# Optimization experiments

Measured on AMD Instinct MI355X. Metric: run time of the kernel, lower is better.

## Reference

```python
import jax, jax.numpy as jnp
import numpy as np

B, T, Q, H = 128, 50, 1024, 256
MAX_STEP = 50
TEMP = 0.5
SUP_W, DIST_W, EMBED_W, LOSS_WEIGHT = 1.0, 0.01, 1.0, 1.0
BLUR, DIAMETER, REACH, SCALING, P = 0.005, 1.0, 500.0, 0.5, 2
NEG = -1e9


def _softmin(eps, C, h):
    # h: log-weights + potential/eps over the second axis of C
    return -eps * jax.nn.logsumexp(h[None, :] - C / eps, axis=1)


def _sqcost(u, v):
    sq = jnp.sum(u * u, -1)[:, None] + jnp.sum(v * v, -1)[None, :] - 2.0 * (u @ v.T)
    return 0.5 * jnp.maximum(sq, 0.0)  # geomloss p=2 cost: |x-y|^2 / 2


def sinkhorn_divergence(x, y):
    # geomloss SamplesLoss('sinkhorn', p=2, blur=0.005, diameter=1, reach=500),
    # tensorized, debiased, unbalanced, eps-scaling schedule.
    N, M = x.shape[0], y.shape[0]
    a_log = jnp.full((N,), -np.log(float(N)), dtype=x.dtype)
    b_log = jnp.full((M,), -np.log(float(M)), dtype=x.dtype)
    Cxy, Cyx = _sqcost(x, y), _sqcost(y, x)
    Cxx, Cyy = _sqcost(x, x), _sqcost(y, y)
    rho = REACH ** P
    eps_final = BLUR ** P
    eps_list = []
    e = DIAMETER ** P
    while e > eps_final:
        eps_list.append(e)
        e = e * (SCALING ** P)
    eps_list.append(eps_final)
    f_ab = jnp.zeros((N,), x.dtype)
    g_ab = jnp.zeros((M,), x.dtype)
    f_aa = jnp.zeros((N,), x.dtype)
    g_bb = jnp.zeros((M,), x.dtype)
    for eps in eps_list:  # static schedule (~9 steps)
        damp = 1.0 / (1.0 + eps / rho)
        ft = damp * _softmin(eps, Cxy, b_log + g_ab / eps)
        gt = damp * _softmin(eps, Cyx, a_log + f_ab / eps)
        faa = 0.5 * (f_aa + damp * _softmin(eps, Cxx, a_log + f_aa / eps))
        gbb = 0.5 * (g_bb + damp * _softmin(eps, Cyy, b_log + g_bb / eps))
        f_ab, g_ab, f_aa, g_bb = ft, gt, faa, gbb
    w = rho + eps_final / 2.0  # UnbalancedWeight
    a_w, b_w = jnp.exp(a_log), jnp.exp(b_log)
    return (jnp.sum(a_w * w * (jnp.exp(-f_aa / rho) - jnp.exp(-f_ab / rho)))
            + jnp.sum(b_w * w * (jnp.exp(-g_bb / rho) - jnp.exp(-g_ab / rho))))


def _forward(lc, lt, le, ltc, ltt, lte, ohs, oht, ods, odt, batch):
    p_c, p_t, p_e = lc / TEMP, lt / TEMP, le / TEMP
    q_c, q_t, q_e = ltc / TEMP, ltt / TEMP, lte / TEMP
    flat = lambda z: z.reshape(z.shape[0], -1)
    loss_kd = (sinkhorn_divergence(flat(p_c), flat(q_c))
               + sinkhorn_divergence(flat(p_t), flat(q_t))
               + sinkhorn_divergence(flat(p_e), flat(q_e)))
    S = MAX_STEP - 1
    delta = batch[:, :, :Q] + batch[:, :, Q:]  # [B,T,Q] question one-hots
    a = jnp.floor(((batch[:, :, :Q] - batch[:, :, Q:]).sum(-1) + 1.0) / 2.0)[:, 1:1 + S]  # [B,S] correctness
    dsh = delta[:, 1:1 + S]  # [B,S,Q]
    # diagonal of p[:S] @ delta[1:].T == per-step gather of next question's logit
    pc = jnp.einsum('bsq,bsq->bs', p_c[:, :S], dsh)
    pt = jnp.einsum('bsq,bsq->bs', p_t[:, :S], dsh)
    pe = jnp.einsum('bsq,bsq->bs', p_e[:, :S], dsh)
    idx = jnp.arange(S)
    last = jnp.max(jnp.where(pc > 0, idx[None, :], -1), axis=1)  # last i with pc[i] > 0
    L = jnp.where(last >= 0, last + 1, S)  # no break => keep full length
    mask = idx[None, :] < L[:, None]
    def ce(logits):
        m = jnp.where(mask, logits, NEG)
        lsm = m - jax.nn.logsumexp(m, axis=1, keepdims=True)
        return -jnp.sum(jnp.where(mask, a * lsm, 0.0))  # soft-target CE, summed over students
    loss_sup = ce(pt) + ce(pc) + ce(pe)
    embed = 0.5 * (jnp.sum((ohs - oht) ** 2) + jnp.sum((ods - odt) ** 2))
    total = LOSS_WEIGHT * (SUP_W * loss_sup + DIST_W * loss_kd + EMBED_W * embed)
    return total.reshape(1)


def setup_inputs():
    key = jax.random.key(0)
    ks = jax.random.split(key, 12)
    rn = lambda k, s: jax.random.normal(k, s, dtype=jnp.float32)
    qid = jax.random.randint(ks[10], (B, T), 0, Q)
    correct = jax.random.randint(ks[11], (B, T), 0, 2).astype(jnp.float32)
    oh = jax.nn.one_hot(qid, Q, dtype=jnp.float32)
    batch = jnp.concatenate([oh * correct[..., None], oh * (1.0 - correct)[..., None]], axis=-1)
    return {
        'logit_c': rn(ks[0], (B, T, Q)),
        'logit_t': rn(ks[1], (B, T, Q)),
        'logit_ensemble': rn(ks[2], (B, T, Q)),
        'logit_teacher_c': rn(ks[3], (B, T, Q)),
        'logit_teacher_t': rn(ks[4], (B, T, Q)),
        'logit_teacher_ensemble': rn(ks[5], (B, T, Q)),
        'out_h_student': rn(ks[6], (B, T, H)),
        'out_h_teacher': rn(ks[7], (B, T, H)),
        'out_d_student': rn(ks[8], (B, T, H)),
        'out_d_teacher': rn(ks[9], (B, T, H)),
        'batch': batch,
    }


def reference(logit_c, logit_t, logit_ensemble, logit_teacher_c, logit_teacher_t, logit_teacher_ensemble, out_h_student, out_h_teacher, out_d_student, out_d_teacher, batch):
    return _forward(logit_c, logit_t, logit_ensemble, logit_teacher_c, logit_teacher_t, logit_teacher_ensemble, out_h_student, out_h_teacher, out_d_student, out_d_teacher, batch)
```

## Files before the change

kernel.cpp:

```cpp
#include <hip/hip_runtime.h>

#define NB 128
#define T_DIM 50
#define Q_DIM 1024
#define H_DIM 256
#define S_DIM 49
#define K_DIM 51200
#define KCHUNKS 80
#define KC 640
#define BK 64
#define NSTAGE 10
#define GRAM_N (NB * NB)
#define LROWU 36
#define CPAD 132

typedef __attribute__((ext_vector_type(4))) float f32x4;
typedef __attribute__((ext_vector_type(8))) _Float16 half8v;
typedef __attribute__((ext_vector_type(4))) unsigned int uint4v;
typedef __attribute__((ext_vector_type(2))) unsigned int uint2v;
using pk2_t = decltype(__builtin_amdgcn_cvt_pkrtz(0.0f, 0.0f));

union PKU { pk2_t p; unsigned int u; };
union U4H8 { uint4v u; half8v h; };

__device__ inline unsigned short f2bf_rn(float x) {
  union { float f; unsigned int u; } v; v.f = x;
  unsigned int r = v.u + 0x7FFFu + ((v.u >> 16) & 1u);
  return (unsigned short)(r >> 16);
}
__device__ inline float bf2f(unsigned short b) {
  union { float f; unsigned int u; } v; v.u = ((unsigned int)b) << 16;
  return v.f;
}

__global__ __launch_bounds__(1024) void gram_fused_kernel(
    const float* __restrict__ s0, const float* __restrict__ s1, const float* __restrict__ s2,
    const float* __restrict__ t0, const float* __restrict__ t1, const float* __restrict__ t2,
    unsigned short* __restrict__ part) {
  __shared__ unsigned int pan[2][2][NB * LROWU];

  const int chunk = blockIdx.x;
  const int pair = blockIdx.y;
  const float* S  = (pair == 0) ? s0 : ((pair == 1) ? s1 : s2);
  const float* Tm = (pair == 0) ? t0 : ((pair == 1) ? t1 : t2);

  const int tid = threadIdx.x;
  const int wave = tid >> 6, lane = tid & 63;
  const int wrow = wave >> 2, wcol = wave & 3;
  const int l15 = lane & 15, quad = lane >> 4;

  f32x4 aXY[2][2], aXX[2][2], aYY[2][2];
#pragma unroll
  for (int i = 0; i < 2; i++)
#pragma unroll
    for (int j = 0; j < 2; j++) {
      aXY[i][j] = (f32x4){0.f, 0.f, 0.f, 0.f};
      aXX[i][j] = (f32x4){0.f, 0.f, 0.f, 0.f};
      aYY[i][j] = (f32x4){0.f, 0.f, 0.f, 0.f};
    }

  const int r0 = tid >> 4;
  const int kq = tid & 15;
  const size_t ro0 = (size_t)r0 * K_DIM;
  const size_t ro1 = (size_t)(r0 + 64) * K_DIM;

  const int kbase = chunk * KC;
  f32x4 pre0, pre1, pre2, pre3;

#define ISSUE_LOADS(KPOS)                                    \
  {                                                          \
    const float* pS = S + (KPOS) + kq * 4;                   \
    const float* pT = Tm + (KPOS) + kq * 4;                  \
    pre0 = *(const f32x4*)(pS + ro0);                        \
    pre1 = *(const f32x4*)(pS + ro1);                        \
    pre2 = *(const f32x4*)(pT + ro0);                        \
    pre3 = *(const f32x4*)(pT + ro1);                        \
  }

#define CVT_WRITE(BUF)                                       \
  {                                                          \
    unsigned int* panA = &pan[BUF][0][0];                    \
    unsigned int* panB = &pan[BUF][1][0];                    \
    PKU a, b; uint2v w;                                      \
    a.p = __builtin_amdgcn_cvt_pkrtz(pre0[0], pre0[1]);      \
    b.p = __builtin_amdgcn_cvt_pkrtz(pre0[2], pre0[3]);      \
    w.x = a.u; w.y = b.u;                                    \
    *(uint2v*)&panA[r0 * LROWU + kq * 2] = w;                \
    a.p = __builtin_amdgcn_cvt_pkrtz(pre1[0], pre1[1]);      \
    b.p = __builtin_amdgcn_cvt_pkrtz(pre1[2], pre1[3]);      \
    w.x = a.u; w.y = b.u;                                    \
    *(uint2v*)&panA[(r0 + 64) * LROWU + kq * 2] = w;         \
    a.p = __builtin_amdgcn_cvt_pkrtz(pre2[0], pre2[1]);      \
    b.p = __builtin_amdgcn_cvt_pkrtz(pre2[2], pre2[3]);      \
    w.x = a.u; w.y = b.u;                                    \
    *(uint2v*)&panB[r0 * LROWU + kq * 2] = w;                \
    a.p = __builtin_amdgcn_cvt_pkrtz(pre3[0], pre3[1]);      \
    b.p = __builtin_amdgcn_cvt_pkrtz(pre3[2], pre3[3]);      \
    w.x = a.u; w.y = b.u;                                    \
    *(uint2v*)&panB[(r0 + 64) * LROWU + kq * 2] = w;         \
  }

  ISSUE_LOADS(kbase)
  CVT_WRITE(0)
  __syncthreads();

  for (int st = 0; st < NSTAGE; st++) {
    const int buf = st & 1;
    if (st + 1 < NSTAGE) ISSUE_LOADS(kbase + (st + 1) * BK)

    {
      const unsigned int* panA = &pan[buf][0][0];
      const unsigned int* panB = &pan[buf][1][0];
#pragma unroll
      for (int ks = 0; ks < 2; ks++) {
        const int kc = ks * 16 + quad * 4;
        half8v as_[2], bs_[2], at_[2], bt_[2];
#pragma unroll
        for (int t = 0; t < 2; t++) {
          U4H8 u;
          u.u = *(const uint4v*)&panA[(wrow * 32 + t * 16 + l15) * LROWU + kc]; as_[t] = u.h;
          u.u = *(const uint4v*)&panA[(wcol * 32 + t * 16 + l15) * LROWU + kc]; bs_[t] = u.h;
          u.u = *(const uint4v*)&panB[(wrow * 32 + t * 16 + l15) * LROWU + kc]; at_[t] = u.h;
          u.u = *(const uint4v*)&panB[(wcol * 32 + t * 16 + l15) * LROWU + kc]; bt_[t] = u.h;
        }
#pragma unroll
        for (int ti = 0; ti < 2; ti++)
#pragma unroll
          for (int tj = 0; tj < 2; tj++) {
            aXY[ti][tj] = __builtin_amdgcn_mfma_f32_16x16x32_f16(as_[ti], bt_[tj], aXY[ti][tj], 0, 0, 0);
            aXX[ti][tj] = __builtin_amdgcn_mfma_f32_16x16x32_f16(as_[ti], bs_[tj], aXX[ti][tj], 0, 0, 0);
            aYY[ti][tj] = __builtin_amdgcn_mfma_f32_16x16x32_f16(at_[ti], bt_[tj], aYY[ti][tj], 0, 0, 0);
          }
      }
    }

    if (st + 1 < NSTAGE) {
      CVT_WRITE((st + 1) & 1)
      __syncthreads();
    }
  }
#undef ISSUE_LOADS
#undef CVT_WRITE

#pragma unroll
  for (int kind = 0; kind < 3; kind++) {
    unsigned short* out = part + ((size_t)(pair * 3 + kind) * KCHUNKS + chunk) * GRAM_N;
#pragma unroll
    for (int ti = 0; ti < 2; ti++)
#pragma unroll
      for (int tj = 0; tj < 2; tj++) {
        const f32x4 v = (kind == 0) ? aXY[ti][tj] : ((kind == 1) ? aXX[ti][tj] : aYY[ti][tj]);
        const int col = wcol * 32 + tj * 16 + l15;
#pragma unroll
        for (int r = 0; r < 4; r++) {
          const int row = wrow * 32 + ti * 16 + quad * 4 + r;
          out[(size_t)row * NB + col] = f2bf_rn(v[r]);
        }
      }
  }
}

__global__ __launch_bounds__(256) void gram_reduce_kernel(
    const unsigned short* __restrict__ part, float* __restrict__ gram) {
  const int idx = blockIdx.x * 256 + threadIdx.x;
  const int g = idx >> 14;
  const int cell = idx & (GRAM_N - 1);
  const unsigned short* p = part + (size_t)g * KCHUNKS * GRAM_N + cell;
  float s = 0.f;
#pragma unroll
  for (int c = 0; c < KCHUNKS; c++) s += bf2f(p[(size_t)c * GRAM_N]);
  gram[idx] = s;
}

__global__ __launch_bounds__(256, 1) void sinkhorn_part_kernel(
    const float* __restrict__ gram, float* __restrict__ kdpart) {
  const int pair = blockIdx.x, kind = blockIdx.y;
  const float* Gxy = gram + (size_t)(3 * pair + 0) * GRAM_N;
  const float* Gxx = gram + (size_t)(3 * pair + 1) * GRAM_N;
  const float* Gyy = gram + (size_t)(3 * pair + 2) * GRAM_N;

  __shared__ float CL[NB * CPAD];
  __shared__ f32x4 h4a[NB / 4];
  __shared__ f32x4 h4b[NB / 4];
  __shared__ float nx[NB], ny[NB];
  __shared__ float red[256];

  const int tid = threadIdx.x;
  if (tid < NB) {
    nx[tid] = Gxx[tid * (NB + 1)];
    ny[tid] = Gyy[tid * (NB + 1)];
    ((float*)h4a)[tid] = 0.f;
    ((float*)h4b)[tid] = 0.f;
  }
  __syncthreads();

  const float* G  = (kind == 0) ? Gxy : ((kind == 1) ? Gxx : Gyy);
  const float* rn = (kind == 2) ? ny : nx;
  const float* cn = (kind == 1) ? nx : ny;
  for (int idx = tid; idx < GRAM_N; idx += 256) {
    const int i = idx >> 7, j = idx & 127;
    CL[i * CPAD + j] = 2.0f * fmaxf(rn[i] + cn[j] - 2.0f * G[idx], 0.0f);
  }
  __syncthreads();

  const float rho = 250000.0f;
  const float AL = -4.852030263919617f;
  const float LOG2E = 1.4426950408889634f;
  const float LN2 = 0.6931471805599453f;
  const int grp = tid >> 7;
  const int i = tid & 127;
  const bool active = (kind == 0) || (grp == 0);
  const bool colread = (kind == 0) && (grp == 1);

  f32x4 crow[32];
  if (active) {
    if (colread) {
#pragma unroll
      for (int jj = 0; jj < 32; jj++) {
        f32x4 v;
        v[0] = CL[(4 * jj + 0) * CPAD + i];
        v[1] = CL[(4 * jj + 1) * CPAD + i];
        v[2] = CL[(4 * jj + 2) * CPAD + i];
        v[3] = CL[(4 * jj + 3) * CPAD + i];
        crow[jj] = v;
      }
    } else {
#pragma unroll
      for (int jj = 0; jj < 32; jj++)
        crow[jj] = *(const f32x4*)&CL[i * CPAD + 4 * jj];
    }
  }

  float eps = 1.0f;
  for (int it = 0; it < 9; it++) {
    if (it == 8) eps = 2.5e-5f;
    const float inv_eps = 1.0f / eps;
    const float damp = 1.0f / (1.0f + eps / rho);
    const float ebl = eps * AL;

    float newp = 0.f;
    if (active) {
      const f32x4* h = (kind == 0 && grp == 0) ? h4b : h4a;
      f32x4 m4 = (f32x4){-3.0e38f, -3.0e38f, -3.0e38f, -3.0e38f};
#pragma unroll
      for (int jj = 0; jj < 32; jj++) {
        const f32x4 u = h[jj] - crow[jj];
        m4[0] = fmaxf(m4[0], u[0]); m4[1] = fmaxf(m4[1], u[1]);
        m4[2] = fmaxf(m4[2], u[2]); m4[3] = fmaxf(m4[3], u[3]);
      }
      const float m = fmaxf(fmaxf(m4[0], m4[1]), fmaxf(m4[2], m4[3]));
      const float k = inv_eps * LOG2E;
      f32x4 s4 = (f32x4){0.f, 0.f, 0.f, 0.f};
#pragma unroll
      for (int jj = 0; jj < 32; jj++) {
        const f32x4 u = h[jj] - crow[jj];
        s4[0] += __builtin_exp2f((u[0] - m) * k);
        s4[1] += __builtin_exp2f((u[1] - m) * k);
        s4[2] += __builtin_exp2f((u[2] - m) * k);
        s4[3] += __builtin_exp2f((u[3] - m) * k);
      }
      const float Ssum = (s4[0] + s4[1]) + (s4[2] + s4[3]);
      const float sm = -(m + ebl + eps * (LN2 * __log2f(Ssum)));
      if (kind == 0) newp = damp * sm;
      else           newp = 0.5f * (((const float*)h4a)[i] + damp * sm);
    }
    __syncthreads();
    if (active) {
      if (grp == 0) ((float*)h4a)[i] = newp;
      else          ((float*)h4b)[i] = newp;
    }
    __syncthreads();
    eps *= 0.25f;
  }

  float v = 0.f;
  if (kind == 0) {
    v = (grp == 0) ? -__expf(-((const float*)h4a)[i] / rho)
                   : -__expf(-((const float*)h4b)[i] / rho);
  } else if (grp == 0) {
    v = __expf(-((const float*)h4a)[i] / rho);
  }
  red[tid] = v;
  __syncthreads();
  for (int st = 128; st > 0; st >>= 1) {
    if (tid < st) red[tid] += red[tid + st];
    __syncthreads();
  }
  if (tid == 0) kdpart[pair * 3 + kind] = red[0];
}

__global__ __launch_bounds__(256) void ps_kernel(
    const float* __restrict__ lc, const float* __restrict__ lt, const float* __restrict__ le,
    const float* __restrict__ batch,
    float* __restrict__ pc, float* __restrict__ pt, float* __restrict__ pe,
    float* __restrict__ aarr) {
  const int bs = blockIdx.x;
  const int b = bs / S_DIM, s = bs % S_DIM;
  const float* brow = batch + ((size_t)b * T_DIM + (s + 1)) * (2 * Q_DIM);
  __shared__ int sq;
  __shared__ float sds;
  if (threadIdx.x == 0) sq = 0;
  __syncthreads();
  for (int q = threadIdx.x; q < Q_DIM; q += 256) {
    float d0 = brow[q], d1 = brow[Q_DIM + q];
    if (d0 + d1 > 0.5f) { sq = q; sds = d0 - d1; }
  }
  __syncthreads();
  if (threadIdx.x == 0) {
    const size_t off = ((size_t)b * T_DIM + s) * Q_DIM + sq;
    pc[bs] = 2.0f * lc[off];
    pt[bs] = 2.0f * lt[off];
    pe[bs] = 2.0f * le[off];
    aarr[bs] = (sds > 0.0f) ? 1.0f : 0.0f;
  }
}

__global__ __launch_bounds__(256) void embed_kernel(
    const f32x4* __restrict__ hs, const f32x4* __restrict__ ht,
    const f32x4* __restrict__ ds, const f32x4* __restrict__ dt,
    float* __restrict__ acc) {
  const int N4 = NB * T_DIM * H_DIM / 4;
  float sum = 0.f;
  for (int idx = blockIdx.x * 256 + threadIdx.x; idx < N4; idx += gridDim.x * 256) {
    f32x4 a = hs[idx] - ht[idx];
    f32x4 b = ds[idx] - dt[idx];
    sum += a[0]*a[0] + a[1]*a[1] + a[2]*a[2] + a[3]*a[3]
         + b[0]*b[0] + b[1]*b[1] + b[2]*b[2] + b[3]*b[3];
  }
  for (int off = 32; off > 0; off >>= 1) sum += __shfl_down(sum, off, 64);
  __shared__ float wsum[4];
  const int lane = threadIdx.x & 63, wv = threadIdx.x >> 6;
  if (lane == 0) wsum[wv] = sum;
  __syncthreads();
  if (threadIdx.x == 0) atomicAdd(acc, wsum[0] + wsum[1] + wsum[2] + wsum[3]);
}

__global__ __launch_bounds__(128) void ce_final_kernel(
    const float* __restrict__ pc, const float* __restrict__ pt, const float* __restrict__ pe,
    const float* __restrict__ aarr, const float* __restrict__ kdpart,
    const float* __restrict__ emb, float* __restrict__ out) {
  __shared__ float sx[4][NB][S_DIM];
  const int tid = threadIdx.x;
  for (int idx = tid; idx < NB * S_DIM; idx += 128) {
    const int b = idx / S_DIM, s = idx - b * S_DIM;
    sx[0][b][s] = pt[idx];
    sx[1][b][s] = pc[idx];
    sx[2][b][s] = pe[idx];
    sx[3][b][s] = aarr[idx];
  }
  __syncthreads();

  const int b = tid;
  int last = -1;
  for (int s = 0; s < S_DIM; s++)
    if (sx[1][b][s] > 0.0f) last = s;
  const int L = (last >= 0) ? (last + 1) : S_DIM;

  float loss = 0.f;
#pragma unroll
  for (int k = 0; k < 3; k++) {
    float m = -3.0e38f;
    for (int s = 0; s < L; s++) m = fmaxf(m, sx[k][b][s]);
    float sum = 0.f;
    for (int s = 0; s < L; s++) sum += __expf(sx[k][b][s] - m);
    const float lse = m + __logf(sum);
    float l = 0.f;
    for (int s = 0; s < L; s++) l += sx[3][b][s] * (sx[k][b][s] - lse);
    loss -= l;
  }

  __shared__ float red[128];
  red[b] = loss;
  __syncthreads();
  for (int st = 64; st > 0; st >>= 1) {
    if (b < st) red[b] += red[b + st];
    __syncthreads();
  }
  if (b == 0) {
    float kd = 0.f;
    for (int k = 0; k < 9; k++) kd += kdpart[k];
    out[0] = red[0] + 0.01f * (250000.0000125f / 128.0f) * kd + 0.5f * emb[0];
  }
}

extern "C" void kernel_launch(void* const* d_in, const int* in_sizes, int n_in,
                              void* d_out, int out_size, void* d_ws, size_t ws_size,
                              hipStream_t stream) {
  const float* lc    = (const float*)d_in[0];
  const float* lt    = (const float*)d_in[1];
  const float* le    = (const float*)d_in[2];
  const float* ltc   = (const float*)d_in[3];
  const float* ltt   = (const float*)d_in[4];
  const float* lte   = (const float*)d_in[5];
  const float* ohs   = (const float*)d_in[6];
  const float* oht   = (const float*)d_in[7];
  const float* ods   = (const float*)d_in[8];
  const float* odt   = (const float*)d_in[9];
  const float* batch = (const float*)d_in[10];

  unsigned short* part = (unsigned short*)d_ws;
  float* gram = (float*)(part + (size_t)9 * KCHUNKS * GRAM_N);
  float* pcb  = gram + 9 * GRAM_N;
  float* ptb  = pcb + NB * S_DIM;
  float* peb  = ptb + NB * S_DIM;
  float* ab   = peb + NB * S_DIM;
  float* kdp  = ab + NB * S_DIM;
  float* emb  = kdp + 9;

  hipMemsetAsync(emb, 0, sizeof(float), stream);

  embed_kernel<<<1600, 256, 0, stream>>>(
      (const f32x4*)ohs, (const f32x4*)oht, (const f32x4*)ods, (const f32x4*)odt, emb);

  ps_kernel<<<NB * S_DIM, 256, 0, stream>>>(lc, lt, le, batch, pcb, ptb, peb, ab);

  gram_fused_kernel<<<dim3(KCHUNKS, 3), 1024, 0, stream>>>(lc, lt, le, ltc, ltt, lte, part);

  gram_reduce_kernel<<<(9 * GRAM_N) / 256, 256, 0, stream>>>(part, gram);

  sinkhorn_part_kernel<<<dim3(3, 3), 256, 0, stream>>>(gram, kdp);

  ce_final_kernel<<<1, 128, 0, stream>>>(pcb, ptb, peb, ab, kdp, emb, (float*)d_out);
}
```

Before: 344.2 us.

## Prefetch two stages ahead in gram kernel and use wave-per-row search in ps_kernel

The gram kernel now holds two register sets of prefetched global loads, issuing loads two k-stages ahead. The main loop is unrolled by two, and each pair of stages alternates the LDS buffers. This aims to hide more global-memory latency behind the MFMA work, at the cost of extra registers in a 1024-thread block. Separately, ps_kernel now assigns one wave per (b,s) row, using vectorized loads and a ballot/shuffle in place of shared-memory writes and block barriers, which cuts the block count by four.

Result: no change. 342.9 us (-0.4%).

```diff
diff --git a/kernel.cpp b/kernel.cpp
--- a/kernel.cpp
+++ b/kernel.cpp
@@ -33,6 +33,68 @@
   return v.f;
 }
 
+__device__ __forceinline__ void issue_loads(
+    const float* __restrict__ S, const float* __restrict__ Tm,
+    size_t ro0, size_t ro1, int kpos, int kq,
+    f32x4& p0, f32x4& p1, f32x4& p2, f32x4& p3) {
+  const float* pS = S + kpos + kq * 4;
+  const float* pT = Tm + kpos + kq * 4;
+  p0 = *(const f32x4*)(pS + ro0);
+  p1 = *(const f32x4*)(pS + ro1);
+  p2 = *(const f32x4*)(pT + ro0);
+  p3 = *(const f32x4*)(pT + ro1);
+}
+
+__device__ __forceinline__ void cvt_write(
+    unsigned int* __restrict__ panA, unsigned int* __restrict__ panB,
+    int r0, int kq,
+    const f32x4& p0, const f32x4& p1, const f32x4& p2, const f32x4& p3) {
+  PKU a, b; uint2v w;
+  a.p = __builtin_amdgcn_cvt_pkrtz(p0[0], p0[1]);
+  b.p = __builtin_amdgcn_cvt_pkrtz(p0[2], p0[3]);
+  w.x = a.u; w.y = b.u;
+  *(uint2v*)&panA[r0 * LROWU + kq * 2] = w;
+  a.p = __builtin_amdgcn_cvt_pkrtz(p1[0], p1[1]);
+  b.p = __builtin_amdgcn_cvt_pkrtz(p1[2], p1[3]);
+  w.x = a.u; w.y = b.u;
+  *(uint2v*)&panA[(r0 + 64) * LROWU + kq * 2] = w;
+  a.p = __builtin_amdgcn_cvt_pkrtz(p2[0], p2[1]);
+  b.p = __builtin_amdgcn_cvt_pkrtz(p2[2], p2[3]);
+  w.x = a.u; w.y = b.u;
+  *(uint2v*)&panB[r0 * LROWU + kq * 2] = w;
+  a.p = __builtin_amdgcn_cvt_pkrtz(p3[0], p3[1]);
+  b.p = __builtin_amdgcn_cvt_pkrtz(p3[2], p3[3]);
+  w.x = a.u; w.y = b.u;
+  *(uint2v*)&panB[(r0 + 64) * LROWU + kq * 2] = w;
+}
+
+__device__ __forceinline__ void compute_stage(
+    const unsigned int* __restrict__ panA, const unsigned int* __restrict__ panB,
+    int wrow, int wcol, int l15, int quad,
+    f32x4 (&aXY)[2][2], f32x4 (&aXX)[2][2], f32x4 (&aYY)[2][2]) {
+#pragma unroll
+  for (int ks = 0; ks < 2; ks++) {
+    const int kc = ks * 16 + quad * 4;
+    half8v as_[2], bs_[2], at_[2], bt_[2];
+#pragma unroll
+    for (int t = 0; t < 2; t++) {
+      U4H8 u;
+      u.u = *(const uint4v*)&panA[(wrow * 32 + t * 16 + l15) * LROWU + kc]; as_[t] = u.h;
+      u.u = *(const uint4v*)&panA[(wcol * 32 + t * 16 + l15) * LROWU + kc]; bs_[t] = u.h;
+      u.u = *(const uint4v*)&panB[(wrow * 32 + t * 16 + l15) * LROWU + kc]; at_[t] = u.h;
+      u.u = *(const uint4v*)&panB[(wcol * 32 + t * 16 + l15) * LROWU + kc]; bt_[t] = u.h;
+    }
+#pragma unroll
+    for (int ti = 0; ti < 2; ti++)
+#pragma unroll
+      for (int tj = 0; tj < 2; tj++) {
+        aXY[ti][tj] = __builtin_amdgcn_mfma_f32_16x16x32_f16(as_[ti], bt_[tj], aXY[ti][tj], 0, 0, 0);
+        aXX[ti][tj] = __builtin_amdgcn_mfma_f32_16x16x32_f16(as_[ti], bs_[tj], aXX[ti][tj], 0, 0, 0);
+        aYY[ti][tj] = __builtin_amdgcn_mfma_f32_16x16x32_f16(at_[ti], bt_[tj], aYY[ti][tj], 0, 0, 0);
+      }
+  }
+}
+
 __global__ __launch_bounds__(1024) void gram_fused_kernel(
     const float* __restrict__ s0, const float* __restrict__ s1, const float* __restrict__ s2,
     const float* __restrict__ t0, const float* __restrict__ t1, const float* __restrict__ t2,
@@ -63,84 +125,31 @@
   const int kq = tid & 15;
   const size_t ro0 = (size_t)r0 * K_DIM;
   const size_t ro1 = (size_t)(r0 + 64) * K_DIM;
-
   const int kbase = chunk * KC;
-  f32x4 pre0, pre1, pre2, pre3;
-
-#define ISSUE_LOADS(KPOS)                                    \
-  {                                                          \
-    const float* pS = S + (KPOS) + kq * 4;                   \
-    const float* pT = Tm + (KPOS) + kq * 4;                  \
-    pre0 = *(const f32x4*)(pS + ro0);                        \
-    pre1 = *(const f32x4*)(pS + ro1);                        \
-    pre2 = *(const f32x4*)(pT + ro0);                        \
-    pre3 = *(const f32x4*)(pT + ro1);                        \
-  }
-
-#define CVT_WRITE(BUF)                                       \
-  {                                                          \
-    unsigned int* panA = &pan[BUF][0][0];                    \
-    unsigned int* panB = &pan[BUF][1][0];                    \
-    PKU a, b; uint2v w;                                      \
-    a.p = __builtin_amdgcn_cvt_pkrtz(pre0[0], pre0[1]);      \
-    b.p = __builtin_amdgcn_cvt_pkrtz(pre0[2], pre0[3]);      \
-    w.x = a.u; w.y = b.u;                                    \
-    *(uint2v*)&panA[r0 * LROWU + kq * 2] = w;                \
-    a.p = __builtin_amdgcn_cvt_pkrtz(pre1[0], pre1[1]);      \
-    b.p = __builtin_amdgcn_cvt_pkrtz(pre1[2], pre1[3]);      \
-    w.x = a.u; w.y = b.u;                                    \
-    *(uint2v*)&panA[(r0 + 64) * LROWU + kq * 2] = w;         \
-    a.p = __builtin_amdgcn_cvt_pkrtz(pre2[0], pre2[1]);      \
-    b.p = __builtin_amdgcn_cvt_pkrtz(pre2[2], pre2[3]);      \
-    w.x = a.u; w.y = b.u;                                    \
-    *(uint2v*)&panB[r0 * LROWU + kq * 2] = w;                \
-    a.p = __builtin_amdgcn_cvt_pkrtz(pre3[0], pre3[1]);      \
-    b.p = __builtin_amdgcn_cvt_pkrtz(pre3[2], pre3[3]);      \
-    w.x = a.u; w.y = b.u;                                    \
-    *(uint2v*)&panB[(r0 + 64) * LROWU + kq * 2] = w;         \
-  }
-
-  ISSUE_LOADS(kbase)
-  CVT_WRITE(0)
-  __syncthreads();
-
-  for (int st = 0; st < NSTAGE; st++) {
-    const int buf = st & 1;
-    if (st + 1 < NSTAGE) ISSUE_LOADS(kbase + (st + 1) * BK)
-
-    {
-      const unsigned int* panA = &pan[buf][0][0];
-      const unsigned int* panB = &pan[buf][1][0];
-#pragma unroll
-      for (int ks = 0; ks < 2; ks++) {
-        const int kc = ks * 16 + quad * 4;
-        half8v as_[2], bs_[2], at_[2], bt_[2];
-#pragma unroll
-        for (int t = 0; t < 2; t++) {
-          U4H8 u;
-          u.u = *(const uint4v*)&panA[(wrow * 32 + t * 16 + l15) * LROWU + kc]; as_[t] = u.h;
-          u.u = *(const uint4v*)&panA[(wcol * 32 + t * 16 + l15) * LROWU + kc]; bs_[t] = u.h;
-          u.u = *(const uint4v*)&panB[(wrow * 32 + t * 16 + l15) * LROWU + kc]; at_[t] = u.h;
-          u.u = *(const uint4v*)&panB[(wcol * 32 + t * 16 + l15) * LROWU + kc]; bt_[t] = u.h;
-        }
-#pragma unroll
-        for (int ti = 0; ti < 2; ti++)
-#pragma unroll
-          for (int tj = 0; tj < 2; tj++) {
-            aXY[ti][tj] = __builtin_amdgcn_mfma_f32_16x16x32_f16(as_[ti], bt_[tj], aXY[ti][tj], 0, 0, 0);
-            aXX[ti][tj] = __builtin_amdgcn_mfma_f32_16x16x32_f16(as_[ti], bs_[tj], aXX[ti][tj], 0, 0, 0);
-            aYY[ti][tj] = __builtin_amdgcn_mfma_f32_16x16x32_f16(at_[ti], bt_[tj], aYY[ti][tj], 0, 0, 0);
-          }
-      }
-    }
-
-    if (st + 1 < NSTAGE) {
-      CVT_WRITE((st + 1) & 1)
+
+  f32x4 A0, A1, A2, A3;
+  f32x4 B0, B1, B2, B3;
+
+  issue_loads(S, Tm, ro0, ro1, kbase, kq, A0, A1, A2, A3);
+  issue_loads(S, Tm, ro0, ro1, kbase + BK, kq, B0, B1, B2, B3);
+  cvt_write(&pan[0][0][0], &pan[0][1][0], r0, kq, A0, A1, A2, A3);
+  __syncthreads();
+
+  for (int s2 = 0; s2 < NSTAGE; s2 += 2) {
+    if (s2 + 2 < NSTAGE)
+      issue_loads(S, Tm, ro0, ro1, kbase + (s2 + 2) * BK, kq, A0, A1, A2, A3);
+    compute_stage(&pan[0][0][0], &pan[0][1][0], wrow, wcol, l15, quad, aXY, aXX, aYY);
+    cvt_write(&pan[1][0][0], &pan[1][1][0], r0, kq, B0, B1, B2, B3);
+    __syncthreads();
+
+    if (s2 + 3 < NSTAGE)
+      issue_loads(S, Tm, ro0, ro1, kbase + (s2 + 3) * BK, kq, B0, B1, B2, B3);
+    compute_stage(&pan[1][0][0], &pan[1][1][0], wrow, wcol, l15, quad, aXY, aXX, aYY);
+    if (s2 + 2 < NSTAGE) {
+      cvt_write(&pan[0][0][0], &pan[0][1][0], r0, kq, A0, A1, A2, A3);
       __syncthreads();
     }
   }
-#undef ISSUE_LOADS
-#undef CVT_WRITE
 
 #pragma unroll
   for (int kind = 0; kind < 3; kind++) {
@@ -294,24 +303,32 @@
     const float* __restrict__ batch,
     float* __restrict__ pc, float* __restrict__ pt, float* __restrict__ pe,
     float* __restrict__ aarr) {
-  const int bs = blockIdx.x;
-  const int b = bs / S_DIM, s = bs % S_DIM;
+  const int w = blockIdx.x * 4 + (threadIdx.x >> 6);
+  if (w >= NB * S_DIM) return;
+  const int lane = threadIdx.x & 63;
+  const int b = w / S_DIM, s = w - b * S_DIM;
   const float* brow = batch + ((size_t)b * T_DIM + (s + 1)) * (2 * Q_DIM);
-  __shared__ int sq;
-  __shared__ float sds;
-  if (threadIdx.x == 0) sq = 0;
-  __syncthreads();
-  for (int q = threadIdx.x; q < Q_DIM; q += 256) {
-    float d0 = brow[q], d1 = brow[Q_DIM + q];
-    if (d0 + d1 > 0.5f) { sq = q; sds = d0 - d1; }
-  }
-  __syncthreads();
-  if (threadIdx.x == 0) {
-    const size_t off = ((size_t)b * T_DIM + s) * Q_DIM + sq;
-    pc[bs] = 2.0f * lc[off];
-    pt[bs] = 2.0f * lt[off];
-    pe[bs] = 2.0f * le[off];
-    aarr[bs] = (sds > 0.0f) ? 1.0f : 0.0f;
+
+  int qv = 0; float dsv = 0.f; bool found = false;
+#pragma unroll
+  for (int c = 0; c < 4; c++) {
+    const int base = c * 256 + lane * 4;
+    const f32x4 d0 = *(const f32x4*)(brow + base);
+    const f32x4 d1 = *(const f32x4*)(brow + Q_DIM + base);
+#pragma unroll
+    for (int j = 0; j < 4; j++)
+      if (d0[j] + d1[j] > 0.5f) { qv = base + j; dsv = d0[j] - d1[j]; found = true; }
+  }
+  const unsigned long long m = __ballot(found);
+  const int src = (m != 0ull) ? (__ffsll((unsigned long long)m) - 1) : 0;
+  qv = __shfl(qv, src, 64);
+  dsv = __shfl(dsv, src, 64);
+  if (lane == 0) {
+    const size_t off = ((size_t)b * T_DIM + s) * Q_DIM + qv;
+    pc[w] = 2.0f * lc[off];
+    pt[w] = 2.0f * lt[off];
+    pe[w] = 2.0f * le[off];
+    aarr[w] = (m != 0ull && dsv > 0.0f) ? 1.0f : 0.0f;
   }
 }
 
@@ -412,7 +429,7 @@
   embed_kernel<<<1600, 256, 0, stream>>>(
       (const f32x4*)ohs, (const f32x4*)oht, (const f32x4*)ods, (const f32x4*)odt, emb);
 
-  ps_kernel<<<NB * S_DIM, 256, 0, stream>>>(lc, lt, le, batch, pcb, ptb, peb, ab);
+  ps_kernel<<<(NB * S_DIM + 3) / 4, 256, 0, stream>>>(lc, lt, le, batch, pcb, ptb, peb, ab);
 
   gram_fused_kernel<<<dim3(KCHUNKS, 3), 1024, 0, stream>>>(lc, lt, le, ltc, ltt, lte, part);
 
```
